# Performance work log

Measured on AMD Instinct MI355X. Metric: run time of the kernel, lower is better.

## Reference

```python
import jax, jax.numpy as jnp
import numpy as np

TOP_K = 8
N_GROUPS = 8
TOP_K_GROUPS = 4
ROUTE_SCALE = 2.5


def setup_inputs() -> dict:
    key = jax.random.key(0)
    k1, k2, k3 = jax.random.split(key, 3)
    x = jax.random.normal(k1, (8192, 7168), dtype=jnp.float32)
    weight = jax.random.normal(k2, (256, 7168), dtype=jnp.float32) * 0.02
    bias = jax.random.normal(k3, (256,), dtype=jnp.float32) * 0.1
    return {"x": x, "weight": weight, "bias": bias}


def reference(x, weight, bias):
    n_tokens = x.shape[0]
    n_experts = weight.shape[0]
    # scores: [T, E]
    logits = jnp.einsum('td,ed->te', x, weight)
    scores = jax.nn.sigmoid(logits)
    original_scores = scores
    scores_b = scores + bias  # bias branch (dim == 7168)
    # group-limited routing
    sg = scores_b.reshape(n_tokens, N_GROUPS, n_experts // N_GROUPS)
    # bias is not None -> group score = sum of top-2 within group
    top2, _ = jax.lax.top_k(sg, 2)
    group_scores = top2.sum(axis=-1)  # [T, G]
    _, group_idx = jax.lax.top_k(group_scores, TOP_K_GROUPS)  # [T, Kg]
    keep = jnp.zeros((n_tokens, N_GROUPS), dtype=bool)
    keep = keep.at[jnp.arange(n_tokens)[:, None], group_idx].set(True)
    masked = jnp.where(keep[:, :, None], sg, -jnp.inf).reshape(n_tokens, n_experts)
    # global top-k over masked scores
    _, indices = jax.lax.top_k(masked, TOP_K)  # [T, K]
    weights = jnp.take_along_axis(original_scores, indices, axis=1)
    weights = weights / weights.sum(axis=-1, keepdims=True)  # sigmoid normalization
    weights = weights * ROUTE_SCALE
    return weights.astype(x.dtype), indices
```

## Files before the change

### kernel.cpp

```cpp
#include <hip/hip_runtime.h>
#include <math.h>

#define T_TOKENS 8192
#define NEXP 256
#define DIM 7168
#define NEG_INF (-3.0e38f)

typedef _Float16 f16;
typedef _Float16 f16x8 __attribute__((ext_vector_type(8)));
typedef __fp16 h16x2 __attribute__((ext_vector_type(2)));
typedef float f32x4 __attribute__((ext_vector_type(4)));

#define AS1 __attribute__((address_space(1)))
#define AS3 __attribute__((address_space(3)))

#define WPLANE_BYTES (NEXP * DIM * 2)
#define PART_OFF (2 * WPLANE_BYTES)
#define UNSCALE 5.9604644775390625e-8f

__global__ __launch_bounds__(256) void wconvert(const float* __restrict__ w,
                                                f16* __restrict__ w0p,
                                                f16* __restrict__ w1p) {
    const int i = (blockIdx.x * 256 + threadIdx.x) * 8;
    const f32x4 u0 = *(const f32x4*)(w + i);
    const f32x4 u1 = *(const f32x4*)(w + i + 4);
    float c[8] = {u0[0]*4096.f, u0[1]*4096.f, u0[2]*4096.f, u0[3]*4096.f,
                  u1[0]*4096.f, u1[1]*4096.f, u1[2]*4096.f, u1[3]*4096.f};
    f16x8 h, g;
#pragma unroll
    for (int j = 0; j < 4; ++j) {
        h16x2 hp = __builtin_amdgcn_cvt_pkrtz(c[2*j], c[2*j+1]);
        float r0 = c[2*j]   - (float)hp[0];
        float r1 = c[2*j+1] - (float)hp[1];
        h16x2 gp = __builtin_amdgcn_cvt_pkrtz(r0, r1);
        h[2*j] = (f16)hp[0]; h[2*j+1] = (f16)hp[1];
        g[2*j] = (f16)gp[0]; g[2*j+1] = (f16)gp[1];
    }
    *(f16x8*)(w0p + i) = h;
    *(f16x8*)(w1p + i) = g;
}

__global__ __launch_bounds__(256, 2) void gemm_f16split(
    const float* __restrict__ x, const f16* __restrict__ w0,
    float* __restrict__ part, int ksplit) {
    __shared__ char smem[65536];
    const int tid = threadIdx.x;
    const int lane = tid & 63;
    const int wv = tid >> 6;
    const int bm = blockIdx.x, bn = blockIdx.y, bz = blockIdx.z;
    const int wr = wv >> 1, wc = wv & 1;
    const int l15 = lane & 15, l7 = lane & 7, q4 = lane >> 4;

    const char* xc = (const char*)x;
    const char* wc0 = (const char*)w0;

    int aoff[8], woff[8], ldsA[8], ldsW[8];
#pragma unroll
    for (int i = 0; i < 8; ++i) {
        const int inst = wv * 8 + i;
        const int arow = inst * 4 + (lane >> 4);
        const int t = lane & 15;
        aoff[i] = (int)((((size_t)(bm * 128 + arow) * DIM + (size_t)bz * ksplit) * 4)
                        + (size_t)((t ^ (arow & 7)) * 16));
        ldsA[i] = inst * 1024;
        const int wrow = (inst & 15) * 8 + (lane >> 3);
        woff[i] = (inst >> 4) * WPLANE_BYTES
                + (int)((((size_t)(bn * 128 + wrow) * DIM + (size_t)bz * ksplit) * 2)
                        + (size_t)(((lane & 7) ^ (wrow & 7)) * 16));
        ldsW[i] = 32768 + inst * 1024;
    }

    int offA[2][2], offB[2];
#pragma unroll
    for (int s = 0; s < 2; ++s) {
        offA[s][0] = ((2 * (s * 4 + q4) + 0) ^ l7) * 16;
        offA[s][1] = ((2 * (s * 4 + q4) + 1) ^ l7) * 16;
        offB[s] = ((s * 4 + q4) ^ l7) * 16;
    }
    const int rowA = (wr * 64 + l15) * 256;
    const int rowB = 32768 + (wc * 64 + l15) * 128;

    f32x4 acc[4][4];
#pragma unroll
    for (int m = 0; m < 4; ++m)
#pragma unroll
        for (int n = 0; n < 4; ++n) acc[m][n] = (f32x4){0.f, 0.f, 0.f, 0.f};

    const int niter = ksplit >> 6;
    for (int kt = 0; kt < niter; ++kt) {
#pragma unroll
        for (int i = 0; i < 8; ++i)
            __builtin_amdgcn_global_load_lds((const AS1 void*)(xc + aoff[i]),
                                             (AS3 void*)(smem + ldsA[i]), 16, 0, 0);
#pragma unroll
        for (int i = 0; i < 8; ++i)
            __builtin_amdgcn_global_load_lds((const AS1 void*)(wc0 + woff[i]),
                                             (AS3 void*)(smem + ldsW[i]), 16, 0, 0);
#pragma unroll
        for (int i = 0; i < 8; ++i) { aoff[i] += 256; woff[i] += 128; }
        __syncthreads();

#pragma unroll
        for (int s = 0; s < 2; ++s) {
            f16x8 bf0[4], bf1[4];
#pragma unroll
            for (int n = 0; n < 4; ++n) {
                bf0[n] = *(const f16x8*)(smem + rowB + n * 2048 + offB[s]);
                bf1[n] = *(const f16x8*)(smem + rowB + 16384 + n * 2048 + offB[s]);
            }
#pragma unroll
            for (int m = 0; m < 4; ++m) {
                const f32x4 v0 = *(const f32x4*)(smem + rowA + m * 4096 + offA[s][0]);
                const f32x4 v1 = *(const f32x4*)(smem + rowA + m * 4096 + offA[s][1]);
                float c[8] = {v0[0]*4096.f, v0[1]*4096.f, v0[2]*4096.f, v0[3]*4096.f,
                              v1[0]*4096.f, v1[1]*4096.f, v1[2]*4096.f, v1[3]*4096.f};
                f16x8 a0, a1;
#pragma unroll
                for (int j = 0; j < 4; ++j) {
                    h16x2 hp = __builtin_amdgcn_cvt_pkrtz(c[2*j], c[2*j+1]);
                    float r0 = c[2*j]   - (float)hp[0];
                    float r1 = c[2*j+1] - (float)hp[1];
                    h16x2 gp = __builtin_amdgcn_cvt_pkrtz(r0, r1);
                    a0[2*j] = (f16)hp[0]; a0[2*j+1] = (f16)hp[1];
                    a1[2*j] = (f16)gp[0]; a1[2*j+1] = (f16)gp[1];
                }
#pragma unroll
                for (int n = 0; n < 4; ++n) {
                    acc[m][n] = __builtin_amdgcn_mfma_f32_16x16x32_f16(a0, bf0[n], acc[m][n], 0, 0, 0);
                    acc[m][n] = __builtin_amdgcn_mfma_f32_16x16x32_f16(a1, bf0[n], acc[m][n], 0, 0, 0);
                    acc[m][n] = __builtin_amdgcn_mfma_f32_16x16x32_f16(a0, bf1[n], acc[m][n], 0, 0, 0);
                    acc[m][n] = __builtin_amdgcn_mfma_f32_16x16x32_f16(a1, bf1[n], acc[m][n], 0, 0, 0);
                }
            }
        }
        __syncthreads();
    }

    float* P = part + (size_t)bz * T_TOKENS * NEXP;
    const int orow = bm * 128 + wr * 64 + (lane >> 4) * 4;
    const int ocol = bn * 128 + wc * 64 + l15;
#pragma unroll
    for (int m = 0; m < 4; ++m)
#pragma unroll
        for (int n = 0; n < 4; ++n)
#pragma unroll
            for (int r = 0; r < 4; ++r)
                P[(size_t)(orow + m * 16 + r) * NEXP + ocol + n * 16] = acc[m][n][r];
}

__global__ __launch_bounds__(256) void routing_kernel(const float* __restrict__ part,
                                                      const float* __restrict__ bias,
                                                      float* __restrict__ out, int nsplit) {
    const int lane = threadIdx.x & 63;
    const int t = blockIdx.x * 4 + (threadIdx.x >> 6);

    f32x4 z = {0.f, 0.f, 0.f, 0.f};
    for (int s = 0; s < nsplit; ++s) {
        const f32x4 v = *((const f32x4*)(part + ((size_t)s * T_TOKENS + t) * NEXP) + lane);
        z[0] += v[0]; z[1] += v[1]; z[2] += v[2]; z[3] += v[3];
    }
    const float s0 = 1.0f / (1.0f + expf(-z[0] * UNSCALE));
    const float s1 = 1.0f / (1.0f + expf(-z[1] * UNSCALE));
    const float s2 = 1.0f / (1.0f + expf(-z[2] * UNSCALE));
    const float s3 = 1.0f / (1.0f + expf(-z[3] * UNSCALE));
    const f32x4 bv = *((const f32x4*)bias + lane);
    float sb0 = s0 + bv[0], sb1 = s1 + bv[1], sb2 = s2 + bv[2], sb3 = s3 + bv[3];

    float m1, m2;
    m1 = sb0; m2 = NEG_INF;
    if (sb1 > m1) { m2 = m1; m1 = sb1; } else if (sb1 > m2) m2 = sb1;
    if (sb2 > m1) { m2 = m1; m1 = sb2; } else if (sb2 > m2) m2 = sb2;
    if (sb3 > m1) { m2 = m1; m1 = sb3; } else if (sb3 > m2) m2 = sb3;
#pragma unroll
    for (int off = 1; off < 8; off <<= 1) {
        const float om1 = __shfl_xor(m1, off);
        const float om2 = __shfl_xor(m2, off);
        const float hi = fmaxf(m1, om1);
        const float lo = fminf(m1, om1);
        m2 = fmaxf(lo, fmaxf(m2, om2));
        m1 = hi;
    }
    const float gs = m1 + m2;

    const float g0 = __shfl(gs, 0),  g1 = __shfl(gs, 8),  g2 = __shfl(gs, 16), g3 = __shfl(gs, 24);
    const float g4 = __shfl(gs, 32), g5 = __shfl(gs, 40), g6 = __shfl(gs, 48), g7 = __shfl(gs, 56);

    float t1 = NEG_INF, t2 = NEG_INF, t3 = NEG_INF, t4 = NEG_INF;
    int i1 = 0, i2 = 0, i3 = 0, i4 = 0;
#define INS4(v, gi)                                                         \
    {                                                                       \
        if (v > t1)      { t4=t3;i4=i3; t3=t2;i3=i2; t2=t1;i2=i1; t1=v;i1=gi; } \
        else if (v > t2) { t4=t3;i4=i3; t3=t2;i3=i2; t2=v;i2=gi; }          \
        else if (v > t3) { t4=t3;i4=i3; t3=v;i3=gi; }                       \
        else if (v > t4) { t4=v;i4=gi; }                                    \
    }
    INS4(g0, 0) INS4(g1, 1) INS4(g2, 2) INS4(g3, 3)
    INS4(g4, 4) INS4(g5, 5) INS4(g6, 6) INS4(g7, 7)
#undef INS4
    const int keepmask = (1 << i1) | (1 << i2) | (1 << i3) | (1 << i4);

    const int g = lane >> 3;
    if (!((keepmask >> g) & 1)) { sb0 = NEG_INF; sb1 = NEG_INF; sb2 = NEG_INF; sb3 = NEG_INF; }

    float wval[8];
    int wi[8];
    float wsum = 0.0f;
#pragma unroll
    for (int r = 0; r < 8; r++) {
        float bvv = sb0;
        int bii = (lane << 2);
        if (sb1 > bvv) { bvv = sb1; bii = (lane << 2) | 1; }
        if (sb2 > bvv) { bvv = sb2; bii = (lane << 2) | 2; }
        if (sb3 > bvv) { bvv = sb3; bii = (lane << 2) | 3; }
#pragma unroll
        for (int off = 1; off < 64; off <<= 1) {
            const float ov = __shfl_xor(bvv, off);
            const int oi = __shfl_xor(bii, off);
            if (ov > bvv || (ov == bvv && oi < bii)) { bvv = ov; bii = oi; }
        }
        const int sl = bii & 3;
        const float cand = (sl == 0) ? s0 : (sl == 1) ? s1 : (sl == 2) ? s2 : s3;
        const float ow = __shfl(cand, bii >> 2);
        wval[r] = ow;
        wi[r] = bii;
        wsum += ow;
        if ((bii >> 2) == lane) {
            if (sl == 0) sb0 = NEG_INF;
            else if (sl == 1) sb1 = NEG_INF;
            else if (sl == 2) sb2 = NEG_INF;
            else sb3 = NEG_INF;
        }
    }
    const float scale = 2.5f / wsum;
    if (lane == 0) {
        float* ow8 = out + (size_t)t * 8;
        float* oi8 = out + (size_t)T_TOKENS * 8 + (size_t)t * 8;
#pragma unroll
        for (int r = 0; r < 8; r++) {
            ow8[r] = wval[r] * scale;
            oi8[r] = (float)wi[r];
        }
    }
}

extern "C" void kernel_launch(void* const* d_in, const int* in_sizes, int n_in,
                              void* d_out, int out_size, void* d_ws, size_t ws_size,
                              hipStream_t stream) {
    const float* x = (const float*)d_in[0];
    const float* w = (const float*)d_in[1];
    const float* bias = (const float*)d_in[2];

    f16* w0 = (f16*)d_ws;
    f16* w1 = (f16*)((char*)d_ws + WPLANE_BYTES);
    float* part = (float*)((char*)d_ws + PART_OFF);

    const size_t need4 = (size_t)PART_OFF + 4ull * T_TOKENS * NEXP * 4;
    const int nsplit = (ws_size >= need4) ? 4 : 2;
    const int ksplit = DIM / nsplit;

    wconvert<<<NEXP * DIM / (256 * 8), 256, 0, stream>>>(w, w0, w1);
    gemm_f16split<<<dim3(64, 2, nsplit), 256, 0, stream>>>(x, w0, part, ksplit);
    routing_kernel<<<T_TOKENS / 4, 256, 0, stream>>>(part, bias, (float*)d_out, nsplit);
}
```

Measured before the change: 143.1 us.

## Double-buffer GEMM K-tiles in LDS with halved K step and MFMA priority

Restructures the split-K GEMM main loop to double-buffer shared memory. The K tile is halved to 32 so that two stages fit in the same 64 KB, and the next tile's global-to-LDS loads are issued before computing the current one. A partial vmcnt wait replaces the full barrier-after-load pattern, aiming to overlap memory latency with MFMA work, and s_setprio raises wave priority around the MFMA bursts. In exchange there are twice as many iterations and barriers per tile of work, and the LDS swizzle layouts are rewritten for the narrower tiles.

New measurement: 141.5 us. About the same (-1.2%).

```diff
diff --git a/kernel.cpp b/kernel.cpp
--- a/kernel.cpp
+++ b/kernel.cpp
@@ -40,7 +40,7 @@
     *(f16x8*)(w1p + i) = g;
 }
 
-__global__ __launch_bounds__(256, 2) void gemm_f16split(
+__global__ __launch_bounds__(256, 2) void gemm_f16split_db(
     const float* __restrict__ x, const f16* __restrict__ w0,
     float* __restrict__ part, int ksplit) {
     __shared__ char smem[65536];
@@ -49,36 +49,42 @@
     const int wv = tid >> 6;
     const int bm = blockIdx.x, bn = blockIdx.y, bz = blockIdx.z;
     const int wr = wv >> 1, wc = wv & 1;
-    const int l15 = lane & 15, l7 = lane & 7, q4 = lane >> 4;
+    const int l15 = lane & 15, q4 = lane >> 4;
 
     const char* xc = (const char*)x;
-    const char* wc0 = (const char*)w0;
-
-    int aoff[8], woff[8], ldsA[8], ldsW[8];
-#pragma unroll
-    for (int i = 0; i < 8; ++i) {
-        const int inst = wv * 8 + i;
-        const int arow = inst * 4 + (lane >> 4);
-        const int t = lane & 15;
-        aoff[i] = (int)((((size_t)(bm * 128 + arow) * DIM + (size_t)bz * ksplit) * 4)
-                        + (size_t)((t ^ (arow & 7)) * 16));
-        ldsA[i] = inst * 1024;
-        const int wrow = (inst & 15) * 8 + (lane >> 3);
-        woff[i] = (inst >> 4) * WPLANE_BYTES
-                + (int)((((size_t)(bn * 128 + wrow) * DIM + (size_t)bz * ksplit) * 2)
-                        + (size_t)(((lane & 7) ^ (wrow & 7)) * 16));
-        ldsW[i] = 32768 + inst * 1024;
-    }
-
-    int offA[2][2], offB[2];
-#pragma unroll
-    for (int s = 0; s < 2; ++s) {
-        offA[s][0] = ((2 * (s * 4 + q4) + 0) ^ l7) * 16;
-        offA[s][1] = ((2 * (s * 4 + q4) + 1) ^ l7) * 16;
-        offB[s] = ((s * 4 + q4) ^ l7) * 16;
-    }
-    const int rowA = (wr * 64 + l15) * 256;
-    const int rowB = 32768 + (wc * 64 + l15) * 128;
+    const char* wcp = (const char*)w0;
+
+    int aoff[4], woff[4], ldsA[4], ldsW[4];
+#pragma unroll
+    for (int i = 0; i < 4; ++i) {
+        const int ai = wv * 4 + i;
+        const int ra = ai * 8 + (lane >> 3);
+        const int ua = lane & 7;
+        aoff[i] = (bm * 128 + ra) * (DIM * 4) + bz * (ksplit * 4)
+                + ((ua ^ (ra & 7)) * 16);
+        ldsA[i] = ai * 1024;
+        const int wi_ = wv * 4 + i;
+        const int p = wi_ >> 3;
+        const int rw = (wi_ & 7) * 16 + (lane >> 2);
+        const int uw = lane & 3;
+        woff[i] = p * WPLANE_BYTES + (bn * 128 + rw) * (DIM * 2) + bz * (ksplit * 2)
+                + ((uw ^ ((rw >> 1) & 3)) * 16);
+        ldsW[i] = 16384 + wi_ * 1024;
+    }
+
+    int rA[4][2], rW[4][2];
+#pragma unroll
+    for (int m = 0; m < 4; ++m) {
+        const int r = wr * 64 + m * 16 + l15;
+        rA[m][0] = r * 128 + (((2 * q4 + 0) ^ (r & 7)) * 16);
+        rA[m][1] = r * 128 + (((2 * q4 + 1) ^ (r & 7)) * 16);
+    }
+#pragma unroll
+    for (int n = 0; n < 4; ++n) {
+        const int rw = wc * 64 + n * 16 + l15;
+        rW[n][0] = 16384 + 0    + rw * 64 + ((q4 ^ ((rw >> 1) & 3)) * 16);
+        rW[n][1] = 16384 + 8192 + rw * 64 + ((q4 ^ ((rw >> 1) & 3)) * 16);
+    }
 
     f32x4 acc[4][4];
 #pragma unroll
@@ -86,55 +92,74 @@
 #pragma unroll
         for (int n = 0; n < 4; ++n) acc[m][n] = (f32x4){0.f, 0.f, 0.f, 0.f};
 
-    const int niter = ksplit >> 6;
-    for (int kt = 0; kt < niter; ++kt) {
-#pragma unroll
-        for (int i = 0; i < 8; ++i)
-            __builtin_amdgcn_global_load_lds((const AS1 void*)(xc + aoff[i]),
-                                             (AS3 void*)(smem + ldsA[i]), 16, 0, 0);
-#pragma unroll
-        for (int i = 0; i < 8; ++i)
-            __builtin_amdgcn_global_load_lds((const AS1 void*)(wc0 + woff[i]),
-                                             (AS3 void*)(smem + ldsW[i]), 16, 0, 0);
-#pragma unroll
-        for (int i = 0; i < 8; ++i) { aoff[i] += 256; woff[i] += 128; }
-        __syncthreads();
-
-#pragma unroll
-        for (int s = 0; s < 2; ++s) {
-            f16x8 bf0[4], bf1[4];
-#pragma unroll
-            for (int n = 0; n < 4; ++n) {
-                bf0[n] = *(const f16x8*)(smem + rowB + n * 2048 + offB[s]);
-                bf1[n] = *(const f16x8*)(smem + rowB + 16384 + n * 2048 + offB[s]);
-            }
-#pragma unroll
-            for (int m = 0; m < 4; ++m) {
-                const f32x4 v0 = *(const f32x4*)(smem + rowA + m * 4096 + offA[s][0]);
-                const f32x4 v1 = *(const f32x4*)(smem + rowA + m * 4096 + offA[s][1]);
-                float c[8] = {v0[0]*4096.f, v0[1]*4096.f, v0[2]*4096.f, v0[3]*4096.f,
-                              v1[0]*4096.f, v1[1]*4096.f, v1[2]*4096.f, v1[3]*4096.f};
-                f16x8 a0, a1;
-#pragma unroll
-                for (int j = 0; j < 4; ++j) {
-                    h16x2 hp = __builtin_amdgcn_cvt_pkrtz(c[2*j], c[2*j+1]);
-                    float r0 = c[2*j]   - (float)hp[0];
-                    float r1 = c[2*j+1] - (float)hp[1];
-                    h16x2 gp = __builtin_amdgcn_cvt_pkrtz(r0, r1);
-                    a0[2*j] = (f16)hp[0]; a0[2*j+1] = (f16)hp[1];
-                    a1[2*j] = (f16)gp[0]; a1[2*j+1] = (f16)gp[1];
-                }
-#pragma unroll
-                for (int n = 0; n < 4; ++n) {
-                    acc[m][n] = __builtin_amdgcn_mfma_f32_16x16x32_f16(a0, bf0[n], acc[m][n], 0, 0, 0);
-                    acc[m][n] = __builtin_amdgcn_mfma_f32_16x16x32_f16(a1, bf0[n], acc[m][n], 0, 0, 0);
-                    acc[m][n] = __builtin_amdgcn_mfma_f32_16x16x32_f16(a0, bf1[n], acc[m][n], 0, 0, 0);
-                    acc[m][n] = __builtin_amdgcn_mfma_f32_16x16x32_f16(a1, bf1[n], acc[m][n], 0, 0, 0);
-                }
-            }
-        }
-        __syncthreads();
-    }
+#define STAGE(sb)                                                               \
+    {                                                                           \
+        _Pragma("unroll")                                                       \
+        for (int i = 0; i < 4; ++i)                                             \
+            __builtin_amdgcn_global_load_lds((const AS1 void*)(xc + aoff[i]),   \
+                (AS3 void*)(smem + (sb) + ldsA[i]), 16, 0, 0);                  \
+        _Pragma("unroll")                                                       \
+        for (int i = 0; i < 4; ++i)                                             \
+            __builtin_amdgcn_global_load_lds((const AS1 void*)(wcp + woff[i]),  \
+                (AS3 void*)(smem + (sb) + ldsW[i]), 16, 0, 0);                  \
+        _Pragma("unroll")                                                       \
+        for (int i = 0; i < 4; ++i) { aoff[i] += 128; woff[i] += 64; }          \
+    }
+
+#define COMPUTE(sb)                                                             \
+    {                                                                           \
+        f16x8 bfr[4][2];                                                        \
+        _Pragma("unroll")                                                       \
+        for (int n = 0; n < 4; ++n) {                                           \
+            bfr[n][0] = *(const f16x8*)(smem + (sb) + rW[n][0]);                \
+            bfr[n][1] = *(const f16x8*)(smem + (sb) + rW[n][1]);                \
+        }                                                                       \
+        _Pragma("unroll")                                                       \
+        for (int m = 0; m < 4; ++m) {                                           \
+            const f32x4 v0 = *(const f32x4*)(smem + (sb) + rA[m][0]);           \
+            const f32x4 v1 = *(const f32x4*)(smem + (sb) + rA[m][1]);           \
+            float c[8] = {v0[0]*4096.f, v0[1]*4096.f, v0[2]*4096.f, v0[3]*4096.f,\
+                          v1[0]*4096.f, v1[1]*4096.f, v1[2]*4096.f, v1[3]*4096.f};\
+            f16x8 a0, a1;                                                       \
+            _Pragma("unroll")                                                   \
+            for (int j = 0; j < 4; ++j) {                                       \
+                h16x2 hp = __builtin_amdgcn_cvt_pkrtz(c[2*j], c[2*j+1]);        \
+                float r0 = c[2*j]   - (float)hp[0];                             \
+                float r1 = c[2*j+1] - (float)hp[1];                             \
+                h16x2 gp = __builtin_amdgcn_cvt_pkrtz(r0, r1);                  \
+                a0[2*j] = (f16)hp[0]; a0[2*j+1] = (f16)hp[1];                   \
+                a1[2*j] = (f16)gp[0]; a1[2*j+1] = (f16)gp[1];                   \
+            }                                                                   \
+            __builtin_amdgcn_s_setprio(1);                                      \
+            _Pragma("unroll")                                                   \
+            for (int n = 0; n < 4; ++n) {                                       \
+                acc[m][n] = __builtin_amdgcn_mfma_f32_16x16x32_f16(a0, bfr[n][0], acc[m][n], 0, 0, 0); \
+                acc[m][n] = __builtin_amdgcn_mfma_f32_16x16x32_f16(a1, bfr[n][0], acc[m][n], 0, 0, 0); \
+                acc[m][n] = __builtin_amdgcn_mfma_f32_16x16x32_f16(a0, bfr[n][1], acc[m][n], 0, 0, 0); \
+                acc[m][n] = __builtin_amdgcn_mfma_f32_16x16x32_f16(a1, bfr[n][1], acc[m][n], 0, 0, 0); \
+            }                                                                   \
+            __builtin_amdgcn_s_setprio(0);                                      \
+        }                                                                       \
+    }
+
+    const int niter = ksplit >> 5;
+    STAGE(0);
+    for (int t = 0; t < niter - 1; ++t) {
+        const int cur = (t & 1) * 32768;
+        const int nxt = ((t + 1) & 1) * 32768;
+        STAGE(nxt);
+        asm volatile("s_waitcnt vmcnt(8)" ::: "memory");
+        __builtin_amdgcn_sched_barrier(0);
+        __builtin_amdgcn_s_barrier();
+        COMPUTE(cur);
+        __builtin_amdgcn_s_barrier();
+    }
+    asm volatile("s_waitcnt vmcnt(0)" ::: "memory");
+    __builtin_amdgcn_sched_barrier(0);
+    __builtin_amdgcn_s_barrier();
+    COMPUTE(((niter - 1) & 1) * 32768);
+#undef STAGE
+#undef COMPUTE
 
     float* P = part + (size_t)bz * T_TOKENS * NEXP;
     const int orow = bm * 128 + wr * 64 + (lane >> 4) * 4;
@@ -259,6 +284,6 @@
     const int ksplit = DIM / nsplit;
 
     wconvert<<<NEXP * DIM / (256 * 8), 256, 0, stream>>>(w, w0, w1);
-    gemm_f16split<<<dim3(64, 2, nsplit), 256, 0, stream>>>(x, w0, part, ksplit);
+    gemm_f16split_db<<<dim3(64, 2, nsplit), 256, 0, stream>>>(x, w0, part, ksplit);
     routing_kernel<<<T_TOKENS / 4, 256, 0, stream>>>(part, bias, (float*)d_out, nsplit);
 }
```
